# Performance work log

Measured on AMD Instinct MI355X. Metric: run time of the kernel, lower is better.

## Reference

```python
import jax, jax.numpy as jnp
import numpy as np

N, T, F_IN, F_OUT, E = 20000, 4, 64, 64, 640000


def setup_inputs() -> dict:
    key = jax.random.key(0)
    k1, k2, k3, k4, k5, k6 = jax.random.split(key, 6)
    node_features = jax.random.normal(k1, (N, T, F_IN), dtype=jnp.float32)
    edge_weights = jax.random.uniform(k2, (T, E), dtype=jnp.float32)
    src = jax.random.randint(k3, (E,), 0, N, dtype=jnp.int32)
    dst = jax.random.randint(k4, (E,), 0, N, dtype=jnp.int32)
    W = jax.random.normal(k5, (F_OUT, F_IN), dtype=jnp.float32) / np.sqrt(F_IN)
    b = jax.random.normal(k6, (F_OUT,), dtype=jnp.float32) * 0.01
    return {"node_features": node_features, "edge_weights": edge_weights,
            "src": src, "dst": dst, "W": W, "b": b}


def reference(node_features, edge_weights, src, dst, W, b):
    # u_mul_e: gather source node features and scale by per-edge, per-time weight
    # edge_weights (T, E) -> transposed (E, T) -> broadcast over feature dim
    msg = node_features[src] * edge_weights.T[:, :, None]          # (E, T, F_IN)
    # fn.sum: scatter-sum messages into destination nodes
    h = jax.ops.segment_sum(msg, dst, num_segments=node_features.shape[0])  # (N, T, F_IN)
    # nn.Linear(in_features, out_features)
    return h @ W.T + b                                             # (N, T, F_OUT)
```

## Files before the change

kernel.cpp:

```cpp
#include <hip/hip_runtime.h>

#define N_NODES 20000
#define T_STEPS 4
#define F_DIM   64
#define E_EDGES 640000
#define ROWS    (N_NODES * T_STEPS)
#define ROW_ELEMS (T_STEPS * F_DIM)

#define SCATTER_BLOCKS   2500
#define TRANSFORM_BLOCKS (ROWS / 64)
#define FUSED_BLOCKS     (SCATTER_BLOCKS + TRANSFORM_BLOCKS)
#define OVF_CAP          4096

typedef unsigned long long u64;

__device__ __forceinline__ unsigned short f32_to_bf16_rne(float f) {
    unsigned u = __float_as_uint(f);
    u += 0x7FFFu + ((u >> 16) & 1u);
    return (unsigned short)(u >> 16);
}
__device__ __forceinline__ float bf16_to_f32(unsigned short h) {
    return __uint_as_float((unsigned)h << 16);
}
__device__ __forceinline__ float rec_weight_bf16(const int4& r, int t) {
    const unsigned word = (t & 2) ? (unsigned)r.z : (unsigned)r.y;
    return bf16_to_f32((t & 1) ? (unsigned short)(word >> 16)
                               : (unsigned short)(word & 0xFFFF));
}
__device__ __forceinline__ unsigned quant12(float w) {
    int q = (int)(w * 4096.0f + 0.5f);
    if (q > 4095) q = 4095;
    return (unsigned)q;
}

__global__ __launch_bounds__(256) void fused_build_kernel(
    const float* __restrict__ x, const float* __restrict__ W,
    unsigned short* __restrict__ yb,
    const int* __restrict__ src, const int* __restrict__ dst,
    const float* __restrict__ ew,
    int* __restrict__ cnt, u64* __restrict__ buckets, int cap,
    int4* __restrict__ ovf, int* __restrict__ ovf_cnt)
{
    const int m3 = blockIdx.x % 3;
    if (m3 != 2) {
        const int sidx = (blockIdx.x / 3) * 2 + m3;
        const int e    = sidx * 256 + threadIdx.x;
        const int d  = dst[e];
        const int s  = src[e];
        const float w0 = ew[e];
        const float w1 = ew[E_EDGES + e];
        const float w2 = ew[2 * E_EDGES + e];
        const float w3 = ew[3 * E_EDGES + e];
        const u64 pack = (u64)(unsigned)s
                       | ((u64)quant12(w0) << 15)
                       | ((u64)quant12(w1) << 27)
                       | ((u64)quant12(w2) << 39)
                       | ((u64)quant12(w3) << 51);
        const int pos = atomicAdd(&cnt[d], 1);
        if (pos < cap) {
            __builtin_nontemporal_store(pack, &buckets[(size_t)d * cap + pos]);
        } else {
            const int o = atomicAdd(ovf_cnt, 1);
            if (o < OVF_CAP) {
                int4 rec;
                rec.x = s;
                rec.y = (unsigned)f32_to_bf16_rne(w0) |
                        ((unsigned)f32_to_bf16_rne(w1) << 16);
                rec.z = (unsigned)f32_to_bf16_rne(w2) |
                        ((unsigned)f32_to_bf16_rne(w3) << 16);
                rec.w = d;
                ovf[o] = rec;
            }
        }
        return;
    }

    __shared__ float xs[64 * 68];
    __shared__ float wt[64 * 68];
    const int tid  = threadIdx.x;
    const int row0 = (blockIdx.x / 3) * 64;

    {
        const int o  = tid & 63;
        const int fb = (tid >> 6) * 16;
#pragma unroll
        for (int k = 0; k < 16; ++k) {
            const int f = fb + k;
            wt[f * 68 + o] = W[o * 64 + f];
        }
    }
    {
        const float4* xg = (const float4*)(x + (size_t)row0 * 64);
#pragma unroll
        for (int k = 0; k < 4; ++k) {
            const int q  = k * 256 + tid;
            const int r  = q >> 4;
            const int c4 = (q & 15) * 4;
            *(float4*)&xs[r * 68 + c4] = xg[q];
        }
    }
    __syncthreads();

    const int rg = tid >> 4;
    const int oq = (tid & 15) * 4;

    float acc[4][4];
#pragma unroll
    for (int i = 0; i < 4; ++i)
#pragma unroll
        for (int j = 0; j < 4; ++j) acc[i][j] = 0.0f;

    for (int f = 0; f < 64; ++f) {
        const float4 w4 = *(const float4*)&wt[f * 68 + oq];
#pragma unroll
        for (int i = 0; i < 4; ++i) {
            const float xv = xs[(rg * 4 + i) * 68 + f];
            acc[i][0] += xv * w4.x;
            acc[i][1] += xv * w4.y;
            acc[i][2] += xv * w4.z;
            acc[i][3] += xv * w4.w;
        }
    }

    const int node = (row0 >> 2) + rg;
#pragma unroll
    for (int i = 0; i < 4; ++i) {
        ushort4 h;
        h.x = f32_to_bf16_rne(acc[i][0]);
        h.y = f32_to_bf16_rne(acc[i][1]);
        h.z = f32_to_bf16_rne(acc[i][2]);
        h.w = f32_to_bf16_rne(acc[i][3]);
        *(ushort4*)(yb + ((size_t)i * N_NODES + node) * 64 + oq) = h;
    }
}

__global__ __launch_bounds__(256) void accumulate_kernel(
    const unsigned short* __restrict__ yb, const int* __restrict__ cnt,
    const u64* __restrict__ buckets, int cap,
    const int4* __restrict__ ovf, const int* __restrict__ ovf_cnt,
    const float* __restrict__ b, float* __restrict__ out)
{
    const int lane  = threadIdx.x & 63;
    const int wv    = threadIdx.x >> 6;
    const int t     = blockIdx.x & 3;
    const int nbase = (blockIdx.x >> 2) * 16 + wv * 4;
    const int g     = lane >> 4;
    const int m     = lane & 15;
    const int sh    = 15 + 12 * t;
    const unsigned short* yt = yb + (size_t)t * N_NODES * 64;
    const float4 bv = *(const float4*)(b + m * 4);

#pragma unroll
    for (int j = 0; j < 4; ++j) {
        const int n     = nbase + j;
        const int total = cnt[n];
        const int deg   = (total > cap) ? cap : total;
        const u64* rp   = buckets + (size_t)n * cap;

        float a0 = 0.f, a1 = 0.f, a2 = 0.f, a3 = 0.f;

        int k = 0;
        for (; k + 16 <= deg; k += 16) {
            u64 p[4];
#pragma unroll
            for (int i = 0; i < 4; ++i) p[i] = rp[k + 4 * i + g];
            uint2 v[4];
#pragma unroll
            for (int i = 0; i < 4; ++i)
                v[i] = *(const uint2*)(yt + (size_t)(unsigned)(p[i] & 0x7FFF) * 64 + m * 4);
#pragma unroll
            for (int i = 0; i < 4; ++i) {
                const float w = (float)(unsigned)((p[i] >> sh) & 0xFFF) * (1.0f / 4096.0f);
                a0 += __uint_as_float(v[i].x << 16) * w;
                a1 += __uint_as_float(v[i].x & 0xFFFF0000u) * w;
                a2 += __uint_as_float(v[i].y << 16) * w;
                a3 += __uint_as_float(v[i].y & 0xFFFF0000u) * w;
            }
        }
        while (k < deg) {
            const int idx  = k + g;
            const bool val = (idx < deg);
            const u64 p    = rp[val ? idx : (deg - 1)];
            const float w  = val ? ((float)(unsigned)((p >> sh) & 0xFFF) * (1.0f / 4096.0f))
                                 : 0.f;
            const uint2 v  = *(const uint2*)(yt + (size_t)(unsigned)(p & 0x7FFF) * 64 + m * 4);
            a0 += __uint_as_float(v.x << 16) * w;
            a1 += __uint_as_float(v.x & 0xFFFF0000u) * w;
            a2 += __uint_as_float(v.y << 16) * w;
            a3 += __uint_as_float(v.y & 0xFFFF0000u) * w;
            k += 4;
        }

        if (total > cap) {
            int mm = *ovf_cnt;
            if (mm > OVF_CAP) mm = OVF_CAP;
            if (g == 0) {
                for (int i = 0; i < mm; ++i) {
                    const int4 r = ovf[i];
                    if (r.w != n) continue;
                    const float w = rec_weight_bf16(r, t);
                    const uint2 v = *(const uint2*)(yt + (size_t)r.x * 64 + m * 4);
                    a0 += __uint_as_float(v.x << 16) * w;
                    a1 += __uint_as_float(v.x & 0xFFFF0000u) * w;
                    a2 += __uint_as_float(v.y << 16) * w;
                    a3 += __uint_as_float(v.y & 0xFFFF0000u) * w;
                }
            }
        }

        a0 += __shfl_xor(a0, 16); a0 += __shfl_xor(a0, 32);
        a1 += __shfl_xor(a1, 16); a1 += __shfl_xor(a1, 32);
        a2 += __shfl_xor(a2, 16); a2 += __shfl_xor(a2, 32);
        a3 += __shfl_xor(a3, 16); a3 += __shfl_xor(a3, 32);

        if (g == 0) {
            float4 o;
            o.x = a0 + bv.x; o.y = a1 + bv.y; o.z = a2 + bv.z; o.w = a3 + bv.w;
            *(float4*)(out + (size_t)n * ROW_ELEMS + t * F_DIM + m * 4) = o;
        }
    }
}

extern "C" void kernel_launch(void* const* d_in, const int* in_sizes, int n_in,
                              void* d_out, int out_size, void* d_ws, size_t ws_size,
                              hipStream_t stream) {
    const float* x   = (const float*)d_in[0];
    const float* ew  = (const float*)d_in[1];
    const int*   src = (const int*)  d_in[2];
    const int*   dst = (const int*)  d_in[3];
    const float* W   = (const float*)d_in[4];
    const float* b   = (const float*)d_in[5];
    float*       out = (float*)d_out;

    char* ws = (char*)d_ws;
    size_t off = 0;
    auto alloc = [&](size_t bytes) {
        void* p = ws + off;
        off += (bytes + 255) & ~(size_t)255;
        return p;
    };
    unsigned short* yb  = (unsigned short*)alloc((size_t)ROWS * 64 * 2);
    int*            cnt = (int*) alloc((N_NODES + 1) * sizeof(int));
    int4*           ovf = (int4*)alloc((size_t)OVF_CAP * sizeof(int4));
    int*            ovf_cnt = cnt + N_NODES;

    size_t rem = (ws_size > off) ? (ws_size - off) : 0;
    int cap = (int)(rem / ((size_t)N_NODES * sizeof(u64)));
    if (cap > 128) cap = 128;
    if (cap < 1) cap = 1;
    u64* buckets = (u64*)(ws + off);

    hipMemsetAsync(cnt, 0, (N_NODES + 1) * sizeof(int), stream);
    fused_build_kernel<<<FUSED_BLOCKS, 256, 0, stream>>>(
        x, W, yb, src, dst, ew, cnt, buckets, cap, ovf, ovf_cnt);
    accumulate_kernel<<<(N_NODES / 16) * T_STEPS, 256, 0, stream>>>(
        yb, cnt, buckets, cap, ovf, ovf_cnt, b, out);
}
```

Measured before the change: 183.8 us.

## Merge build and accumulate into one persistent kernel with a grid barrier

Replaces the two launches with a single persistent kernel of 256 blocks × 1024 threads. It runs the edge bucketing and the node transform in a grid-stride loop, then synchronises all blocks through an atomic-counter spin barrier before the gather-accumulate phase. The yb layout changes to node-major so one wave handles all four time steps of a node per edge, which removes the cross-group shuffle reduction. The aim is to cut launch overhead and get wider reads per edge. In exchange the barrier depends on all 256 blocks being co-resident, there is less parallelism at 256 blocks, and per-wave work is serialised over the full degree.

```diff
diff --git a/kernel.cpp b/kernel.cpp
--- a/kernel.cpp
+++ b/kernel.cpp
@@ -7,10 +7,11 @@
 #define ROWS    (N_NODES * T_STEPS)
 #define ROW_ELEMS (T_STEPS * F_DIM)
 
-#define SCATTER_BLOCKS   2500
-#define TRANSFORM_BLOCKS (ROWS / 64)
-#define FUSED_BLOCKS     (SCATTER_BLOCKS + TRANSFORM_BLOCKS)
-#define OVF_CAP          4096
+#define GRID_BLOCKS  256
+#define BLOCK_THR    1024
+#define PHASE1_VB    1250
+#define PHASE2_VB    1250
+#define OVF_CAP      4096
 
 typedef unsigned long long u64;
 
@@ -33,191 +34,197 @@
     return (unsigned)q;
 }
 
-__global__ __launch_bounds__(256) void fused_build_kernel(
-    const float* __restrict__ x, const float* __restrict__ W,
-    unsigned short* __restrict__ yb,
+__global__ __launch_bounds__(BLOCK_THR, 4) void mega_kernel(
+    const float* __restrict__ x, const float* __restrict__ ew,
     const int* __restrict__ src, const int* __restrict__ dst,
-    const float* __restrict__ ew,
-    int* __restrict__ cnt, u64* __restrict__ buckets, int cap,
-    int4* __restrict__ ovf, int* __restrict__ ovf_cnt)
+    const float* __restrict__ W, const float* __restrict__ b,
+    float* __restrict__ out, unsigned short* __restrict__ yb,
+    int* __restrict__ cnt, int4* __restrict__ ovf,
+    u64* __restrict__ buckets, int cap)
 {
-    const int m3 = blockIdx.x % 3;
-    if (m3 != 2) {
-        const int sidx = (blockIdx.x / 3) * 2 + m3;
-        const int e    = sidx * 256 + threadIdx.x;
-        const int d  = dst[e];
-        const int s  = src[e];
-        const float w0 = ew[e];
-        const float w1 = ew[E_EDGES + e];
-        const float w2 = ew[2 * E_EDGES + e];
-        const float w3 = ew[3 * E_EDGES + e];
-        const u64 pack = (u64)(unsigned)s
-                       | ((u64)quant12(w0) << 15)
-                       | ((u64)quant12(w1) << 27)
-                       | ((u64)quant12(w2) << 39)
-                       | ((u64)quant12(w3) << 51);
-        const int pos = atomicAdd(&cnt[d], 1);
-        if (pos < cap) {
-            __builtin_nontemporal_store(pack, &buckets[(size_t)d * cap + pos]);
+    __shared__ float xs[128 * 68];
+    __shared__ float wt[64 * 68];
+    const int tid = threadIdx.x;
+    int* ovf_cnt = cnt + N_NODES;
+    int* gbar    = cnt + N_NODES + 1;
+
+    for (int vb = blockIdx.x; vb < PHASE1_VB; vb += GRID_BLOCKS) {
+        if ((vb & 1) == 0) {
+            const int e = (vb >> 1) * 1024 + tid;
+            const int d  = dst[e];
+            const int s  = src[e];
+            const float w0 = ew[e];
+            const float w1 = ew[E_EDGES + e];
+            const float w2 = ew[2 * E_EDGES + e];
+            const float w3 = ew[3 * E_EDGES + e];
+            const u64 pack = (u64)(unsigned)s
+                           | ((u64)quant12(w0) << 15)
+                           | ((u64)quant12(w1) << 27)
+                           | ((u64)quant12(w2) << 39)
+                           | ((u64)quant12(w3) << 51);
+            const int pos = atomicAdd(&cnt[d], 1);
+            if (pos < cap) {
+                __builtin_nontemporal_store(pack, &buckets[(size_t)d * cap + pos]);
+            } else {
+                const int o = atomicAdd(ovf_cnt, 1);
+                if (o < OVF_CAP) {
+                    int4 rec;
+                    rec.x = s;
+                    rec.y = (unsigned)f32_to_bf16_rne(w0) |
+                            ((unsigned)f32_to_bf16_rne(w1) << 16);
+                    rec.z = (unsigned)f32_to_bf16_rne(w2) |
+                            ((unsigned)f32_to_bf16_rne(w3) << 16);
+                    rec.w = d;
+                    ovf[o] = rec;
+                }
+            }
         } else {
-            const int o = atomicAdd(ovf_cnt, 1);
-            if (o < OVF_CAP) {
-                int4 rec;
-                rec.x = s;
-                rec.y = (unsigned)f32_to_bf16_rne(w0) |
-                        ((unsigned)f32_to_bf16_rne(w1) << 16);
-                rec.z = (unsigned)f32_to_bf16_rne(w2) |
-                        ((unsigned)f32_to_bf16_rne(w3) << 16);
-                rec.w = d;
-                ovf[o] = rec;
-            }
-        }
-        return;
+            const int row0 = (vb >> 1) * 128;
+            __syncthreads();
+            {
+                const int o  = tid & 63;
+                const int fb = (tid >> 6) * 4;
+#pragma unroll
+                for (int k = 0; k < 4; ++k) {
+                    const int f = fb + k;
+                    wt[f * 68 + o] = W[o * 64 + f];
+                }
+            }
+            {
+                const float4* xg = (const float4*)(x + (size_t)row0 * 64);
+#pragma unroll
+                for (int k = 0; k < 2; ++k) {
+                    const int q  = k * 1024 + tid;
+                    const int r  = q >> 4;
+                    const int c4 = (q & 15) * 4;
+                    *(float4*)&xs[r * 68 + c4] = xg[q];
+                }
+            }
+            __syncthreads();
+
+            const int rg = tid >> 4;
+            const int oq = (tid & 15) * 4;
+
+            float acc[2][4];
+#pragma unroll
+            for (int i = 0; i < 2; ++i)
+#pragma unroll
+                for (int j = 0; j < 4; ++j) acc[i][j] = 0.0f;
+
+            for (int f = 0; f < 64; ++f) {
+                const float4 w4 = *(const float4*)&wt[f * 68 + oq];
+#pragma unroll
+                for (int i = 0; i < 2; ++i) {
+                    const float xv = xs[(rg * 2 + i) * 68 + f];
+                    acc[i][0] += xv * w4.x;
+                    acc[i][1] += xv * w4.y;
+                    acc[i][2] += xv * w4.z;
+                    acc[i][3] += xv * w4.w;
+                }
+            }
+
+#pragma unroll
+            for (int i = 0; i < 2; ++i) {
+                const int r = row0 + rg * 2 + i;
+                ushort4 h;
+                h.x = f32_to_bf16_rne(acc[i][0]);
+                h.y = f32_to_bf16_rne(acc[i][1]);
+                h.z = f32_to_bf16_rne(acc[i][2]);
+                h.w = f32_to_bf16_rne(acc[i][3]);
+                *(ushort4*)(yb + (size_t)r * 64 + oq) = h;
+            }
+        }
     }
 
-    __shared__ float xs[64 * 68];
-    __shared__ float wt[64 * 68];
-    const int tid  = threadIdx.x;
-    const int row0 = (blockIdx.x / 3) * 64;
-
-    {
-        const int o  = tid & 63;
-        const int fb = (tid >> 6) * 16;
-#pragma unroll
-        for (int k = 0; k < 16; ++k) {
-            const int f = fb + k;
-            wt[f * 68 + o] = W[o * 64 + f];
-        }
-    }
-    {
-        const float4* xg = (const float4*)(x + (size_t)row0 * 64);
-#pragma unroll
-        for (int k = 0; k < 4; ++k) {
-            const int q  = k * 256 + tid;
-            const int r  = q >> 4;
-            const int c4 = (q & 15) * 4;
-            *(float4*)&xs[r * 68 + c4] = xg[q];
-        }
+    __syncthreads();
+    if (tid == 0) {
+        __threadfence();
+        atomicAdd(gbar, 1);
+        while (atomicAdd(gbar, 0) < GRID_BLOCKS) {
+            __builtin_amdgcn_s_sleep(2);
+        }
+        __threadfence();
     }
     __syncthreads();
 
-    const int rg = tid >> 4;
-    const int oq = (tid & 15) * 4;
-
-    float acc[4][4];
-#pragma unroll
-    for (int i = 0; i < 4; ++i)
-#pragma unroll
-        for (int j = 0; j < 4; ++j) acc[i][j] = 0.0f;
-
-    for (int f = 0; f < 64; ++f) {
-        const float4 w4 = *(const float4*)&wt[f * 68 + oq];
-#pragma unroll
-        for (int i = 0; i < 4; ++i) {
-            const float xv = xs[(rg * 4 + i) * 68 + f];
-            acc[i][0] += xv * w4.x;
-            acc[i][1] += xv * w4.y;
-            acc[i][2] += xv * w4.z;
-            acc[i][3] += xv * w4.w;
-        }
-    }
-
-    const int node = (row0 >> 2) + rg;
-#pragma unroll
-    for (int i = 0; i < 4; ++i) {
-        ushort4 h;
-        h.x = f32_to_bf16_rne(acc[i][0]);
-        h.y = f32_to_bf16_rne(acc[i][1]);
-        h.z = f32_to_bf16_rne(acc[i][2]);
-        h.w = f32_to_bf16_rne(acc[i][3]);
-        *(ushort4*)(yb + ((size_t)i * N_NODES + node) * 64 + oq) = h;
-    }
-}
-
-__global__ __launch_bounds__(256) void accumulate_kernel(
-    const unsigned short* __restrict__ yb, const int* __restrict__ cnt,
-    const u64* __restrict__ buckets, int cap,
-    const int4* __restrict__ ovf, const int* __restrict__ ovf_cnt,
-    const float* __restrict__ b, float* __restrict__ out)
-{
-    const int lane  = threadIdx.x & 63;
-    const int wv    = threadIdx.x >> 6;
-    const int t     = blockIdx.x & 3;
-    const int nbase = (blockIdx.x >> 2) * 16 + wv * 4;
-    const int g     = lane >> 4;
-    const int m     = lane & 15;
-    const int sh    = 15 + 12 * t;
-    const unsigned short* yt = yb + (size_t)t * N_NODES * 64;
-    const float4 bv = *(const float4*)(b + m * 4);
-
-#pragma unroll
-    for (int j = 0; j < 4; ++j) {
-        const int n     = nbase + j;
+    const int lane = tid & 63;
+    const int wv   = tid >> 6;
+    const int t    = lane >> 4;
+    const int l4   = lane * 4;
+    const int sh   = 15 + 12 * t;
+    const float4 bv = *(const float4*)(b + (lane & 15) * 4);
+
+    for (int vb = blockIdx.x; vb < PHASE2_VB; vb += GRID_BLOCKS) {
+        const int n     = vb * 16 + wv;
         const int total = cnt[n];
         const int deg   = (total > cap) ? cap : total;
         const u64* rp   = buckets + (size_t)n * cap;
 
-        float a0 = 0.f, a1 = 0.f, a2 = 0.f, a3 = 0.f;
+        float4 acc = make_float4(0.f, 0.f, 0.f, 0.f);
 
         int k = 0;
-        for (; k + 16 <= deg; k += 16) {
+        for (; k + 8 <= deg; k += 8) {
+            u64 p[8];
+#pragma unroll
+            for (int i = 0; i < 8; ++i) p[i] = rp[k + i];
+            uint2 v[8];
+#pragma unroll
+            for (int i = 0; i < 8; ++i)
+                v[i] = *(const uint2*)(yb + (size_t)(unsigned)(p[i] & 0x7FFF) * ROW_ELEMS + l4);
+#pragma unroll
+            for (int i = 0; i < 8; ++i) {
+                const float w = (float)(unsigned)((p[i] >> sh) & 0xFFF) * (1.0f / 4096.0f);
+                acc.x += __uint_as_float(v[i].x << 16) * w;
+                acc.y += __uint_as_float(v[i].x & 0xFFFF0000u) * w;
+                acc.z += __uint_as_float(v[i].y << 16) * w;
+                acc.w += __uint_as_float(v[i].y & 0xFFFF0000u) * w;
+            }
+        }
+        if (k + 4 <= deg) {
             u64 p[4];
 #pragma unroll
-            for (int i = 0; i < 4; ++i) p[i] = rp[k + 4 * i + g];
+            for (int i = 0; i < 4; ++i) p[i] = rp[k + i];
             uint2 v[4];
 #pragma unroll
             for (int i = 0; i < 4; ++i)
-                v[i] = *(const uint2*)(yt + (size_t)(unsigned)(p[i] & 0x7FFF) * 64 + m * 4);
+                v[i] = *(const uint2*)(yb + (size_t)(unsigned)(p[i] & 0x7FFF) * ROW_ELEMS + l4);
 #pragma unroll
             for (int i = 0; i < 4; ++i) {
                 const float w = (float)(unsigned)((p[i] >> sh) & 0xFFF) * (1.0f / 4096.0f);
-                a0 += __uint_as_float(v[i].x << 16) * w;
-                a1 += __uint_as_float(v[i].x & 0xFFFF0000u) * w;
-                a2 += __uint_as_float(v[i].y << 16) * w;
-                a3 += __uint_as_float(v[i].y & 0xFFFF0000u) * w;
-            }
-        }
-        while (k < deg) {
-            const int idx  = k + g;
-            const bool val = (idx < deg);
-            const u64 p    = rp[val ? idx : (deg - 1)];
-            const float w  = val ? ((float)(unsigned)((p >> sh) & 0xFFF) * (1.0f / 4096.0f))
-                                 : 0.f;
-            const uint2 v  = *(const uint2*)(yt + (size_t)(unsigned)(p & 0x7FFF) * 64 + m * 4);
-            a0 += __uint_as_float(v.x << 16) * w;
-            a1 += __uint_as_float(v.x & 0xFFFF0000u) * w;
-            a2 += __uint_as_float(v.y << 16) * w;
-            a3 += __uint_as_float(v.y & 0xFFFF0000u) * w;
+                acc.x += __uint_as_float(v[i].x << 16) * w;
+                acc.y += __uint_as_float(v[i].x & 0xFFFF0000u) * w;
+                acc.z += __uint_as_float(v[i].y << 16) * w;
+                acc.w += __uint_as_float(v[i].y & 0xFFFF0000u) * w;
+            }
             k += 4;
+        }
+        for (; k < deg; ++k) {
+            const u64 p   = rp[k];
+            const float w = (float)(unsigned)((p >> sh) & 0xFFF) * (1.0f / 4096.0f);
+            const uint2 v = *(const uint2*)(yb + (size_t)(unsigned)(p & 0x7FFF) * ROW_ELEMS + l4);
+            acc.x += __uint_as_float(v.x << 16) * w;
+            acc.y += __uint_as_float(v.x & 0xFFFF0000u) * w;
+            acc.z += __uint_as_float(v.y << 16) * w;
+            acc.w += __uint_as_float(v.y & 0xFFFF0000u) * w;
         }
 
         if (total > cap) {
             int mm = *ovf_cnt;
             if (mm > OVF_CAP) mm = OVF_CAP;
-            if (g == 0) {
-                for (int i = 0; i < mm; ++i) {
-                    const int4 r = ovf[i];
-                    if (r.w != n) continue;
-                    const float w = rec_weight_bf16(r, t);
-                    const uint2 v = *(const uint2*)(yt + (size_t)r.x * 64 + m * 4);
-                    a0 += __uint_as_float(v.x << 16) * w;
-                    a1 += __uint_as_float(v.x & 0xFFFF0000u) * w;
-                    a2 += __uint_as_float(v.y << 16) * w;
-                    a3 += __uint_as_float(v.y & 0xFFFF0000u) * w;
-                }
-            }
-        }
-
-        a0 += __shfl_xor(a0, 16); a0 += __shfl_xor(a0, 32);
-        a1 += __shfl_xor(a1, 16); a1 += __shfl_xor(a1, 32);
-        a2 += __shfl_xor(a2, 16); a2 += __shfl_xor(a2, 32);
-        a3 += __shfl_xor(a3, 16); a3 += __shfl_xor(a3, 32);
-
-        if (g == 0) {
-            float4 o;
-            o.x = a0 + bv.x; o.y = a1 + bv.y; o.z = a2 + bv.z; o.w = a3 + bv.w;
-            *(float4*)(out + (size_t)n * ROW_ELEMS + t * F_DIM + m * 4) = o;
-        }
+            for (int i = 0; i < mm; ++i) {
+                const int4 r = ovf[i];
+                if (r.w != n) continue;
+                const float w = rec_weight_bf16(r, t);
+                const uint2 v = *(const uint2*)(yb + (size_t)r.x * ROW_ELEMS + l4);
+                acc.x += __uint_as_float(v.x << 16) * w;
+                acc.y += __uint_as_float(v.x & 0xFFFF0000u) * w;
+                acc.z += __uint_as_float(v.y << 16) * w;
+                acc.w += __uint_as_float(v.y & 0xFFFF0000u) * w;
+            }
+        }
+
+        acc.x += bv.x; acc.y += bv.y; acc.z += bv.z; acc.w += bv.w;
+        *(float4*)(out + (size_t)n * ROW_ELEMS + l4) = acc;
     }
 }
 
@@ -240,9 +247,8 @@
         return p;
     };
     unsigned short* yb  = (unsigned short*)alloc((size_t)ROWS * 64 * 2);
-    int*            cnt = (int*) alloc((N_NODES + 1) * sizeof(int));
+    int*            cnt = (int*) alloc((N_NODES + 2) * sizeof(int));
     int4*           ovf = (int4*)alloc((size_t)OVF_CAP * sizeof(int4));
-    int*            ovf_cnt = cnt + N_NODES;
 
     size_t rem = (ws_size > off) ? (ws_size - off) : 0;
     int cap = (int)(rem / ((size_t)N_NODES * sizeof(u64)));
@@ -250,9 +256,7 @@
     if (cap < 1) cap = 1;
     u64* buckets = (u64*)(ws + off);
 
-    hipMemsetAsync(cnt, 0, (N_NODES + 1) * sizeof(int), stream);
-    fused_build_kernel<<<FUSED_BLOCKS, 256, 0, stream>>>(
-        x, W, yb, src, dst, ew, cnt, buckets, cap, ovf, ovf_cnt);
-    accumulate_kernel<<<(N_NODES / 16) * T_STEPS, 256, 0, stream>>>(
-        yb, cnt, buckets, cap, ovf, ovf_cnt, b, out);
-}
+    hipMemsetAsync(cnt, 0, (N_NODES + 2) * sizeof(int), stream);
+    mega_kernel<<<GRID_BLOCKS, BLOCK_THR, 0, stream>>>(
+        x, ew, src, dst, W, b, out, yb, cnt, ovf, buckets, cap);
+}
```

Result: slower. 190.8 us (+3.8%).
